# Kernel optimization log

Measured on AMD Instinct MI355X. Metric: run time of the kernel, lower is better.

Reference implementation:

```python
import jax, jax.numpy as jnp
import numpy as np

D_MODEL = 1024
N_HEADS = 16
HEAD_DIM = D_MODEL // N_HEADS
D_FF = 4096
B, T = 2, 2048


def layernorm(x, g, b, eps=1e-5):
    mu = jnp.mean(x, axis=-1, keepdims=True)
    var = jnp.var(x, axis=-1, keepdims=True)
    return (x - mu) * jax.lax.rsqrt(var + eps) * g + b


def setup_inputs() -> dict:
    key = jax.random.key(0)
    ks = jax.random.split(key, 8)
    s = 0.02
    return {
        "x": jax.random.normal(ks[0], (B, T, D_MODEL), dtype=jnp.float32),
        "ln1_g": jnp.ones((D_MODEL,), jnp.float32),
        "ln1_b": jnp.zeros((D_MODEL,), jnp.float32),
        "qkv_w": jax.random.normal(ks[1], (D_MODEL, 3 * D_MODEL), jnp.float32) * s,
        "qkv_b": jnp.zeros((3 * D_MODEL,), jnp.float32),
        "proj_w": jax.random.normal(ks[2], (D_MODEL, D_MODEL), jnp.float32) * s,
        "proj_b": jnp.zeros((D_MODEL,), jnp.float32),
        "ln2_g": jnp.ones((D_MODEL,), jnp.float32),
        "ln2_b": jnp.zeros((D_MODEL,), jnp.float32),
        "mlp_w1": jax.random.normal(ks[3], (D_MODEL, D_FF), jnp.float32) * s,
        "mlp_b1": jnp.zeros((D_FF,), jnp.float32),
        "mlp_w2": jax.random.normal(ks[4], (D_FF, D_MODEL), jnp.float32) * s,
        "mlp_b2": jnp.zeros((D_MODEL,), jnp.float32),
    }


def reference(x, ln1_g, ln1_b, qkv_w, qkv_b, proj_w, proj_b,
              ln2_g, ln2_b, mlp_w1, mlp_b1, mlp_w2, mlp_b2):
    Bv, Tv, C = x.shape
    scale = HEAD_DIM ** -0.5
    # --- attention branch ---
    h = layernorm(x, ln1_g, ln1_b)
    qkv = h @ qkv_w + qkv_b                                   # [B,T,3C]
    qkv = qkv.reshape(Bv, Tv, 3, N_HEADS, HEAD_DIM)
    q, k, v = qkv[:, :, 0], qkv[:, :, 1], qkv[:, :, 2]        # [B,T,H,Dh]
    att = jnp.einsum('bqhd,bkhd->bhqk', q, k) * scale         # [B,H,T,T]
    causal = jnp.tril(jnp.ones((Tv, Tv), dtype=bool))
    att = jnp.where(causal[None, None], att, -jnp.inf)
    att = jax.nn.softmax(att, axis=-1)
    out = jnp.einsum('bhqk,bkhd->bqhd', att, v).reshape(Bv, Tv, C)
    out = out @ proj_w + proj_b
    x = x + out
    # --- mlp branch ---
    h2 = layernorm(x, ln2_g, ln2_b)
    h2 = jax.nn.gelu(h2 @ mlp_w1 + mlp_b1, approximate=False)
    x = x + (h2 @ mlp_w2 + mlp_b2)
    return x
```

## Files before the change

kernel.cpp:

```cpp
#include <hip/hip_runtime.h>
#include <hip/hip_bf16.h>
#include <cstdint>

typedef __attribute__((ext_vector_type(4))) float f32x4;
typedef __attribute__((ext_vector_type(8))) __bf16 bf16x8;
typedef __attribute__((ext_vector_type(4))) __bf16 bf16x4;

#define EPI_BF16 0
#define EPI_GELU 1
#define EPI_RES  2

__device__ __forceinline__ void gll16(const void* g, void* l) {
  __builtin_amdgcn_global_load_lds((__attribute__((address_space(1))) void*)(g),
                                   (__attribute__((address_space(3))) void*)(l), 16, 0, 0);
}

__global__ __launch_bounds__(256)
void convT(const float* __restrict__ W, __bf16* __restrict__ WT, int Kd, int Nd)
{
  __shared__ __bf16 t[64][72];
  const int tid = threadIdx.x;
  const int n0 = blockIdx.x * 64, k0 = blockIdx.y * 64;
#pragma unroll
  for (int i = 0; i < 4; ++i) {
    const int c = i * 256 + tid;
    const int r = c >> 4, cc = (c & 15) * 4;
    const float4 v = *(const float4*)(W + (size_t)(k0 + r) * Nd + n0 + cc);
    bf16x4 tv; tv[0] = (__bf16)v.x; tv[1] = (__bf16)v.y; tv[2] = (__bf16)v.z; tv[3] = (__bf16)v.w;
    *(bf16x4*)&t[r][cc] = tv;
  }
  __syncthreads();
#pragma unroll
  for (int i = 0; i < 2; ++i) {
    const int c = i * 256 + tid;
    const int n = c >> 3, s = (c & 7) * 8;
    bf16x8 o;
#pragma unroll
    for (int j = 0; j < 8; ++j) o[j] = t[s + j][n];
    *(bf16x8*)(WT + (size_t)(n0 + n) * Kd + k0 + s) = o;
  }
}

__global__ __launch_bounds__(256)
void ln_rows(const float* __restrict__ x, const float* __restrict__ g,
             const float* __restrict__ b, __bf16* __restrict__ out)
{
  const int row = blockIdx.x;
  const int tid = threadIdx.x;
  const float4 v = *(const float4*)(x + (size_t)row * 1024 + tid * 4);
  float s = v.x + v.y + v.z + v.w;
  float q = v.x * v.x + v.y * v.y + v.z * v.z + v.w * v.w;
#pragma unroll
  for (int o = 32; o; o >>= 1) { s += __shfl_xor(s, o); q += __shfl_xor(q, o); }
  __shared__ float red[8];
  const int wid = tid >> 6;
  if ((tid & 63) == 0) { red[wid] = s; red[4 + wid] = q; }
  __syncthreads();
  s = red[0] + red[1] + red[2] + red[3];
  q = red[4] + red[5] + red[6] + red[7];
  const float mu = s * (1.0f / 1024.0f);
  const float var = q * (1.0f / 1024.0f) - mu * mu;
  const float rs = rsqrtf(var + 1e-5f);
  bf16x4 o4;
#pragma unroll
  for (int i = 0; i < 4; ++i) {
    const int c = tid * 4 + i;
    const float xv = (&v.x)[i];
    o4[i] = (__bf16)((xv - mu) * rs * g[c] + b[c]);
  }
  *(bf16x4*)(out + (size_t)row * 1024 + tid * 4) = o4;
}

template<int EPI>
__global__ __launch_bounds__(256)
void gemm_bt(const __bf16* __restrict__ A, const __bf16* __restrict__ BT,
             const float* __restrict__ bias, const float* __restrict__ R,
             void* __restrict__ Out, int M, int N, int K)
{
  const int tid = threadIdx.x;
  const int lane = tid & 63, wid = tid >> 6;
  const int l15 = lane & 15, lg = lane >> 4;
  const int wm = (wid >> 1) * 64, wn = (wid & 1) * 64;
  const int rowBase = blockIdx.y * 128, colBase = blockIdx.x * 128;
  __shared__ __bf16 As[128 * 32];
  __shared__ __bf16 Bs[128 * 32];
  f32x4 acc[4][4] = {};

  for (int k0 = 0; k0 < K; k0 += 32) {
#pragma unroll
    for (int i = 0; i < 2; ++i) {
      const int c = i * 256 + tid;
      const int r = c >> 2, s = (c & 3) * 8;
      gll16(A + (size_t)(rowBase + r) * K + (k0 + s), As + c * 8);
    }
#pragma unroll
    for (int i = 0; i < 2; ++i) {
      const int c = i * 256 + tid;
      const int r = c >> 2, s = (c & 3) * 8;
      gll16(BT + (size_t)(colBase + r) * K + (k0 + s), Bs + c * 8);
    }
    __syncthreads();
    bf16x8 af[4], bfr[4];
#pragma unroll
    for (int m = 0; m < 4; ++m) af[m] = *(const bf16x8*)(As + (wm + m * 16 + l15) * 32 + lg * 8);
#pragma unroll
    for (int n = 0; n < 4; ++n) bfr[n] = *(const bf16x8*)(Bs + (wn + n * 16 + l15) * 32 + lg * 8);
#pragma unroll
    for (int m = 0; m < 4; ++m)
#pragma unroll
      for (int n = 0; n < 4; ++n)
        acc[m][n] = __builtin_amdgcn_mfma_f32_16x16x32_bf16(af[m], bfr[n], acc[m][n], 0, 0, 0);
    __syncthreads();
  }
#pragma unroll
  for (int m = 0; m < 4; ++m) {
#pragma unroll
    for (int n = 0; n < 4; ++n) {
      const int col = colBase + wn + n * 16 + l15;
      const float bb = bias[col];
#pragma unroll
      for (int i = 0; i < 4; ++i) {
        const int row = rowBase + wm + m * 16 + lg * 4 + i;
        float v = acc[m][n][i] + bb;
        if constexpr (EPI == EPI_GELU) {
          v = 0.5f * v * (1.0f + erff(v * 0.70710678118654752f));
          ((__bf16*)Out)[(size_t)row * N + col] = (__bf16)v;
        } else if constexpr (EPI == EPI_BF16) {
          ((__bf16*)Out)[(size_t)row * N + col] = (__bf16)v;
        } else {
          v += R[(size_t)row * N + col];
          ((float*)Out)[(size_t)row * N + col] = v;
        }
      }
    }
  }
}

__global__ __launch_bounds__(256)
void rearrange(const __bf16* __restrict__ qkv, __bf16* __restrict__ Q,
               __bf16* __restrict__ Kb, __bf16* __restrict__ VT)
{
  __shared__ __bf16 vt[64][72];
  const int tid = threadIdx.x;
  const int bid = blockIdx.x;
  const int bh = bid >> 5, tt = bid & 31;
  const int b = bh >> 4, h = bh & 15;
  const int t0 = tt * 64;
#pragma unroll
  for (int i = 0; i < 2; ++i) {
    const int c = i * 256 + tid;
    const int tk = c >> 3, d0 = (c & 7) * 8;
    const size_t srow = (size_t)(b * 2048 + t0 + tk) * 3072 + h * 64 + d0;
    const size_t drow = (size_t)(bh * 2048 + t0 + tk) * 64 + d0;
    *(bf16x8*)(Q + drow) = *(const bf16x8*)(qkv + srow);
    *(bf16x8*)(Kb + drow) = *(const bf16x8*)(qkv + srow + 1024);
    *(bf16x8*)&vt[tk][d0] = *(const bf16x8*)(qkv + srow + 2048);
  }
  __syncthreads();
#pragma unroll
  for (int i = 0; i < 2; ++i) {
    const int c = i * 256 + tid;
    const int d = c >> 3, s = (c & 7) * 8;
    bf16x8 o;
#pragma unroll
    for (int j = 0; j < 8; ++j) o[j] = vt[s + j][d];
    *(bf16x8*)(VT + (size_t)(bh * 64 + d) * 2048 + t0 + s) = o;
  }
}

__global__ __launch_bounds__(256)
void attn(const __bf16* __restrict__ Q, const __bf16* __restrict__ K,
          const __bf16* __restrict__ VT, __bf16* __restrict__ O)
{
  const int bid = blockIdx.x;
  const int bh = bid >> 5, qt = bid & 31;
  const int tid = threadIdx.x;
  const int lane = tid & 63, w = tid >> 6;
  const int l15 = lane & 15, lg = lane >> 4;
  __shared__ __bf16 Ks[64 * 64];
  __shared__ __bf16 Vs[64 * 64];
  __shared__ __bf16 Ps[4][16 * 72];
  const size_t base = (size_t)bh * 2048 * 64;
  const int qrow0 = qt * 64 + w * 16;
  bf16x8 aq[2];
#pragma unroll
  for (int kk = 0; kk < 2; ++kk)
    aq[kk] = *(const bf16x8*)(Q + base + (size_t)(qrow0 + l15) * 64 + kk * 32 + lg * 8);
  f32x4 oacc[4] = {};
  float mst[4], lst[4];
#pragma unroll
  for (int i = 0; i < 4; ++i) { mst[i] = -INFINITY; lst[i] = 0.0f; }

  const int xsw = (l15 & 7) << 3;

  for (int j = 0; j <= qt; ++j) {
#pragma unroll
    for (int i = 0; i < 2; ++i) {
      const int c = i * 256 + tid;
      const int r = c >> 3;
      const int sc = ((c & 7) ^ (r & 7)) * 8;
      gll16(K + base + (size_t)(j * 64 + r) * 64 + sc, Ks + c * 8);
      gll16(VT + base + (size_t)r * 2048 + j * 64 + sc, Vs + c * 8);
    }
    __syncthreads();
    f32x4 sf[4];
#pragma unroll
    for (int n = 0; n < 4; ++n) {
      f32x4 z = {};
#pragma unroll
      for (int kk = 0; kk < 2; ++kk) {
        bf16x8 bk = *(const bf16x8*)(Ks + (n * 16 + l15) * 64 + ((kk * 32 + lg * 8) ^ xsw));
        z = __builtin_amdgcn_mfma_f32_16x16x32_bf16(aq[kk], bk, z, 0, 0, 0);
      }
      sf[n] = z;
    }
    const bool diag = (j == qt);
#pragma unroll
    for (int n = 0; n < 4; ++n)
#pragma unroll
      for (int i = 0; i < 4; ++i) {
        float sv = sf[n][i] * 0.125f;
        if (diag) {
          const int kv = j * 64 + n * 16 + l15;
          const int qr = qrow0 + lg * 4 + i;
          if (kv > qr) sv = -INFINITY;
        }
        sf[n][i] = sv;
      }
    float mx[4], cf[4], rsum[4];
#pragma unroll
    for (int i = 0; i < 4; ++i) {
      float t = fmaxf(fmaxf(sf[0][i], sf[1][i]), fmaxf(sf[2][i], sf[3][i]));
#pragma unroll
      for (int o = 1; o < 16; o <<= 1) t = fmaxf(t, __shfl_xor(t, o));
      mx[i] = fmaxf(t, mst[i]);
      cf[i] = __expf(mst[i] - mx[i]);
      rsum[i] = 0.0f;
    }
#pragma unroll
    for (int n = 0; n < 4; ++n)
#pragma unroll
      for (int i = 0; i < 4; ++i) {
        const float p = __expf(sf[n][i] - mx[i]);
        rsum[i] += p;
        Ps[w][(lg * 4 + i) * 72 + n * 16 + l15] = (__bf16)p;
      }
#pragma unroll
    for (int i = 0; i < 4; ++i) {
      float t = rsum[i];
#pragma unroll
      for (int o = 1; o < 16; o <<= 1) t += __shfl_xor(t, o);
      lst[i] = lst[i] * cf[i] + t;
      mst[i] = mx[i];
    }
#pragma unroll
    for (int n = 0; n < 4; ++n)
#pragma unroll
      for (int i = 0; i < 4; ++i) oacc[n][i] *= cf[i];
#pragma unroll
    for (int t = 0; t < 2; ++t) {
      bf16x8 ap = *(const bf16x8*)(Ps[w] + l15 * 72 + t * 32 + lg * 8);
#pragma unroll
      for (int n = 0; n < 4; ++n) {
        bf16x8 bv = *(const bf16x8*)(Vs + (n * 16 + l15) * 64 + ((t * 32 + lg * 8) ^ xsw));
        oacc[n] = __builtin_amdgcn_mfma_f32_16x16x32_bf16(ap, bv, oacc[n], 0, 0, 0);
      }
    }
    __syncthreads();
  }
  const int b = bh >> 4, h = bh & 15;
#pragma unroll
  for (int i = 0; i < 4; ++i) {
    const float inv = 1.0f / lst[i];
    const int t = qrow0 + lg * 4 + i;
#pragma unroll
    for (int n = 0; n < 4; ++n)
      O[(size_t)(b * 2048 + t) * 1024 + h * 64 + n * 16 + l15] = (__bf16)(oacc[n][i] * inv);
  }
}

extern "C" void kernel_launch(void* const* d_in, const int* in_sizes, int n_in,
                              void* d_out, int out_size, void* d_ws, size_t ws_size,
                              hipStream_t stream)
{
  const float* x      = (const float*)d_in[0];
  const float* ln1_g  = (const float*)d_in[1];
  const float* ln1_b  = (const float*)d_in[2];
  const float* qkv_w  = (const float*)d_in[3];
  const float* qkv_b  = (const float*)d_in[4];
  const float* proj_w = (const float*)d_in[5];
  const float* proj_b = (const float*)d_in[6];
  const float* ln2_g  = (const float*)d_in[7];
  const float* ln2_b  = (const float*)d_in[8];
  const float* mlp_w1 = (const float*)d_in[9];
  const float* mlp_b1 = (const float*)d_in[10];
  const float* mlp_w2 = (const float*)d_in[11];
  const float* mlp_b2 = (const float*)d_in[12];

  char* ws = (char*)d_ws;
  __bf16* qkvT  = (__bf16*)(ws + 0);
  __bf16* projT = (__bf16*)(ws + 6291456);
  __bf16* w1T   = (__bf16*)(ws + 8388608);
  __bf16* w2T   = (__bf16*)(ws + 16777216);
  __bf16* h1    = (__bf16*)(ws + 25165824);
  __bf16* qkv   = (__bf16*)(ws + 33554432);
  __bf16* act1  = (__bf16*)(ws + 33554432);
  __bf16* Qb    = (__bf16*)(ws + 58720256);
  __bf16* Kb    = (__bf16*)(ws + 67108864);
  __bf16* VTb   = (__bf16*)(ws + 75497472);
  __bf16* attO  = (__bf16*)(ws + 83886080);
  float*  x2    = (float*) (ws + 92274688);
  __bf16* h2    = (__bf16*)(ws + 109051904);

  convT<<<dim3(48, 16), 256, 0, stream>>>(qkv_w, qkvT, 1024, 3072);
  convT<<<dim3(16, 16), 256, 0, stream>>>(proj_w, projT, 1024, 1024);
  convT<<<dim3(64, 16), 256, 0, stream>>>(mlp_w1, w1T, 1024, 4096);
  convT<<<dim3(16, 64), 256, 0, stream>>>(mlp_w2, w2T, 4096, 1024);

  ln_rows<<<4096, 256, 0, stream>>>(x, ln1_g, ln1_b, h1);
  gemm_bt<EPI_BF16><<<dim3(24, 32), 256, 0, stream>>>(h1, qkvT, qkv_b, nullptr, qkv, 4096, 3072, 1024);
  rearrange<<<1024, 256, 0, stream>>>(qkv, Qb, Kb, VTb);
  attn<<<1024, 256, 0, stream>>>(Qb, Kb, VTb, attO);
  gemm_bt<EPI_RES><<<dim3(8, 32), 256, 0, stream>>>(attO, projT, proj_b, x, x2, 4096, 1024, 1024);
  ln_rows<<<4096, 256, 0, stream>>>(x2, ln2_g, ln2_b, h2);
  gemm_bt<EPI_GELU><<<dim3(32, 32), 256, 0, stream>>>(h2, w1T, mlp_b1, nullptr, act1, 4096, 4096, 1024);
  gemm_bt<EPI_RES><<<dim3(8, 32), 256, 0, stream>>>(act1, w2T, mlp_b2, x2, (float*)d_out, 4096, 1024, 4096);
}
```

Baseline: 485.8 us.

## Rewrite attention with 32x32 MFMA, transposed scores and register-resident P

The attention kernel now uses 2 waves of 32 query rows each with 32x32x16 bf16 MFMAs, computing S^T so each lane owns one query row. The softmax max and sum need only a single cross-half shuffle. P stays in registers via packed bf16 conversion and permlane32_swap instead of round-tripping through LDS. Blocks are also issued in reverse query-tile order so the longest causal tiles start first. The aim is to cut LDS traffic, shuffle reductions and instruction count, at the cost of fewer threads per block, more registers per lane, and correctness depending on the exact MFMA lane layout.

```diff
diff --git a/kernel.cpp b/kernel.cpp
--- a/kernel.cpp
+++ b/kernel.cpp
@@ -3,8 +3,11 @@
 #include <cstdint>
 
 typedef __attribute__((ext_vector_type(4))) float f32x4;
+typedef __attribute__((ext_vector_type(16))) float f32x16;
 typedef __attribute__((ext_vector_type(8))) __bf16 bf16x8;
 typedef __attribute__((ext_vector_type(4))) __bf16 bf16x4;
+typedef __attribute__((ext_vector_type(4))) uint32_t u32x4;
+typedef __attribute__((ext_vector_type(2))) unsigned int u32x2;
 
 #define EPI_BF16 0
 #define EPI_GELU 1
@@ -168,114 +171,118 @@
   }
 }
 
-__global__ __launch_bounds__(256)
+__global__ __launch_bounds__(128)
 void attn(const __bf16* __restrict__ Q, const __bf16* __restrict__ K,
           const __bf16* __restrict__ VT, __bf16* __restrict__ O)
 {
   const int bid = blockIdx.x;
-  const int bh = bid >> 5, qt = bid & 31;
+  const int bh = bid >> 5, qt = 31 - (bid & 31);
   const int tid = threadIdx.x;
   const int lane = tid & 63, w = tid >> 6;
-  const int l15 = lane & 15, lg = lane >> 4;
+  const int l31 = lane & 31, hi = lane >> 5;
   __shared__ __bf16 Ks[64 * 64];
   __shared__ __bf16 Vs[64 * 64];
-  __shared__ __bf16 Ps[4][16 * 72];
   const size_t base = (size_t)bh * 2048 * 64;
-  const int qrow0 = qt * 64 + w * 16;
-  bf16x8 aq[2];
-#pragma unroll
-  for (int kk = 0; kk < 2; ++kk)
-    aq[kk] = *(const bf16x8*)(Q + base + (size_t)(qrow0 + l15) * 64 + kk * 32 + lg * 8);
-  f32x4 oacc[4] = {};
-  float mst[4], lst[4];
-#pragma unroll
-  for (int i = 0; i < 4; ++i) { mst[i] = -INFINITY; lst[i] = 0.0f; }
-
-  const int xsw = (l15 & 7) << 3;
+  const int qrow0 = qt * 64 + w * 32;
+  const int xsw = (l31 & 7) << 3;
+
+  bf16x8 qf[4];
+#pragma unroll
+  for (int s = 0; s < 4; ++s)
+    qf[s] = *(const bf16x8*)(Q + base + (size_t)(qrow0 + l31) * 64 + s * 16 + hi * 8);
+
+  f32x16 oa0 = {}, oa1 = {};
+  float mst = -INFINITY, lst = 0.0f;
 
   for (int j = 0; j <= qt; ++j) {
 #pragma unroll
-    for (int i = 0; i < 2; ++i) {
-      const int c = i * 256 + tid;
+    for (int rnd = 0; rnd < 4; ++rnd) {
+      const int c = rnd * 128 + tid;
       const int r = c >> 3;
-      const int sc = ((c & 7) ^ (r & 7)) * 8;
-      gll16(K + base + (size_t)(j * 64 + r) * 64 + sc, Ks + c * 8);
-      gll16(VT + base + (size_t)r * 2048 + j * 64 + sc, Vs + c * 8);
+      const int e = ((c & 7) ^ (r & 7)) * 8;
+      gll16(K + base + (size_t)(j * 64 + r) * 64 + e, Ks + c * 8);
+      gll16(VT + base + (size_t)r * 2048 + j * 64 + e, Vs + c * 8);
     }
     __syncthreads();
-    f32x4 sf[4];
-#pragma unroll
-    for (int n = 0; n < 4; ++n) {
-      f32x4 z = {};
-#pragma unroll
-      for (int kk = 0; kk < 2; ++kk) {
-        bf16x8 bk = *(const bf16x8*)(Ks + (n * 16 + l15) * 64 + ((kk * 32 + lg * 8) ^ xsw));
-        z = __builtin_amdgcn_mfma_f32_16x16x32_bf16(aq[kk], bk, z, 0, 0, 0);
+
+    f32x16 s0v = {}, s1v = {};
+#pragma unroll
+    for (int s = 0; s < 4; ++s) {
+      const int co = (s * 16 + hi * 8) ^ xsw;
+      bf16x8 ak0 = *(const bf16x8*)(Ks + l31 * 64 + co);
+      bf16x8 ak1 = *(const bf16x8*)(Ks + (32 + l31) * 64 + co);
+      s0v = __builtin_amdgcn_mfma_f32_32x32x16_bf16(ak0, qf[s], s0v, 0, 0, 0);
+      s1v = __builtin_amdgcn_mfma_f32_32x32x16_bf16(ak1, qf[s], s1v, 0, 0, 0);
+    }
+#pragma unroll
+    for (int rg = 0; rg < 16; ++rg) { s0v[rg] *= 0.125f; s1v[rg] *= 0.125f; }
+    if (j == qt) {
+      const int qg = qrow0 + l31;
+#pragma unroll
+      for (int rg = 0; rg < 16; ++rg) {
+        const int kr = j * 64 + ((rg & 3) + 8 * (rg >> 2)) + 4 * hi;
+        if (kr > qg) s0v[rg] = -INFINITY;
+        if (kr + 32 > qg) s1v[rg] = -INFINITY;
       }
-      sf[n] = z;
-    }
-    const bool diag = (j == qt);
-#pragma unroll
-    for (int n = 0; n < 4; ++n)
-#pragma unroll
-      for (int i = 0; i < 4; ++i) {
-        float sv = sf[n][i] * 0.125f;
-        if (diag) {
-          const int kv = j * 64 + n * 16 + l15;
-          const int qr = qrow0 + lg * 4 + i;
-          if (kv > qr) sv = -INFINITY;
-        }
-        sf[n][i] = sv;
+    }
+    float mx = s0v[0];
+#pragma unroll
+    for (int rg = 1; rg < 16; ++rg) mx = fmaxf(mx, s0v[rg]);
+#pragma unroll
+    for (int rg = 0; rg < 16; ++rg) mx = fmaxf(mx, s1v[rg]);
+    mx = fmaxf(mx, __shfl_xor(mx, 32));
+    const float mnew = fmaxf(mst, mx);
+    const float cf = __expf(mst - mnew);
+    float rs = 0.0f;
+#pragma unroll
+    for (int rg = 0; rg < 16; ++rg) {
+      s0v[rg] = __expf(s0v[rg] - mnew); rs += s0v[rg];
+      s1v[rg] = __expf(s1v[rg] - mnew); rs += s1v[rg];
+    }
+    rs += __shfl_xor(rs, 32);
+    lst = lst * cf + rs;
+    mst = mnew;
+#pragma unroll
+    for (int rg = 0; rg < 16; ++rg) {
+      const float cb = __shfl(cf, (rg & 3) + 8 * (rg >> 2) + 4 * hi);
+      oa0[rg] *= cb; oa1[rg] *= cb;
+    }
+#pragma unroll
+    for (int s = 0; s < 4; ++s) {
+      const int br = (s & 1) * 8;
+      uint32_t wA0, wA1, wB0, wB1;
+      if (s < 2) {
+        asm("v_cvt_pk_bf16_f32 %0, %1, %2" : "=v"(wA0) : "v"(s0v[br + 0]), "v"(s0v[br + 1]));
+        asm("v_cvt_pk_bf16_f32 %0, %1, %2" : "=v"(wA1) : "v"(s0v[br + 2]), "v"(s0v[br + 3]));
+        asm("v_cvt_pk_bf16_f32 %0, %1, %2" : "=v"(wB0) : "v"(s0v[br + 4]), "v"(s0v[br + 5]));
+        asm("v_cvt_pk_bf16_f32 %0, %1, %2" : "=v"(wB1) : "v"(s0v[br + 6]), "v"(s0v[br + 7]));
+      } else {
+        asm("v_cvt_pk_bf16_f32 %0, %1, %2" : "=v"(wA0) : "v"(s1v[br + 0]), "v"(s1v[br + 1]));
+        asm("v_cvt_pk_bf16_f32 %0, %1, %2" : "=v"(wA1) : "v"(s1v[br + 2]), "v"(s1v[br + 3]));
+        asm("v_cvt_pk_bf16_f32 %0, %1, %2" : "=v"(wB0) : "v"(s1v[br + 4]), "v"(s1v[br + 5]));
+        asm("v_cvt_pk_bf16_f32 %0, %1, %2" : "=v"(wB1) : "v"(s1v[br + 6]), "v"(s1v[br + 7]));
       }
-    float mx[4], cf[4], rsum[4];
-#pragma unroll
-    for (int i = 0; i < 4; ++i) {
-      float t = fmaxf(fmaxf(sf[0][i], sf[1][i]), fmaxf(sf[2][i], sf[3][i]));
-#pragma unroll
-      for (int o = 1; o < 16; o <<= 1) t = fmaxf(t, __shfl_xor(t, o));
-      mx[i] = fmaxf(t, mst[i]);
-      cf[i] = __expf(mst[i] - mx[i]);
-      rsum[i] = 0.0f;
-    }
-#pragma unroll
-    for (int n = 0; n < 4; ++n)
-#pragma unroll
-      for (int i = 0; i < 4; ++i) {
-        const float p = __expf(sf[n][i] - mx[i]);
-        rsum[i] += p;
-        Ps[w][(lg * 4 + i) * 72 + n * 16 + l15] = (__bf16)p;
-      }
-#pragma unroll
-    for (int i = 0; i < 4; ++i) {
-      float t = rsum[i];
-#pragma unroll
-      for (int o = 1; o < 16; o <<= 1) t += __shfl_xor(t, o);
-      lst[i] = lst[i] * cf[i] + t;
-      mst[i] = mx[i];
-    }
-#pragma unroll
-    for (int n = 0; n < 4; ++n)
-#pragma unroll
-      for (int i = 0; i < 4; ++i) oacc[n][i] *= cf[i];
-#pragma unroll
-    for (int t = 0; t < 2; ++t) {
-      bf16x8 ap = *(const bf16x8*)(Ps[w] + l15 * 72 + t * 32 + lg * 8);
-#pragma unroll
-      for (int n = 0; n < 4; ++n) {
-        bf16x8 bv = *(const bf16x8*)(Vs + (n * 16 + l15) * 64 + ((t * 32 + lg * 8) ^ xsw));
-        oacc[n] = __builtin_amdgcn_mfma_f32_16x16x32_bf16(ap, bv, oacc[n], 0, 0, 0);
-      }
+      const u32x2 r0 = __builtin_amdgcn_permlane32_swap(wA0, wB0, false, false);
+      const u32x2 r1 = __builtin_amdgcn_permlane32_swap(wA1, wB1, false, false);
+      u32x4 uu; uu.x = r0.x; uu.y = r1.x; uu.z = r0.y; uu.w = r1.y;
+      const bf16x8 pa = __builtin_bit_cast(bf16x8, uu);
+      const int co = (s * 16 + hi * 8) ^ xsw;
+      bf16x8 bv0 = *(const bf16x8*)(Vs + l31 * 64 + co);
+      bf16x8 bv1 = *(const bf16x8*)(Vs + (32 + l31) * 64 + co);
+      oa0 = __builtin_amdgcn_mfma_f32_32x32x16_bf16(pa, bv0, oa0, 0, 0, 0);
+      oa1 = __builtin_amdgcn_mfma_f32_32x32x16_bf16(pa, bv1, oa1, 0, 0, 0);
     }
     __syncthreads();
   }
-  const int b = bh >> 4, h = bh & 15;
-#pragma unroll
-  for (int i = 0; i < 4; ++i) {
-    const float inv = 1.0f / lst[i];
-    const int t = qrow0 + lg * 4 + i;
-#pragma unroll
-    for (int n = 0; n < 4; ++n)
-      O[(size_t)(b * 2048 + t) * 1024 + h * 64 + n * 16 + l15] = (__bf16)(oacc[n][i] * inv);
+  const float inv = 1.0f / lst;
+  const int b = bh >> 4, hd = bh & 15;
+#pragma unroll
+  for (int rg = 0; rg < 16; ++rg) {
+    const int cr = (rg & 3) + 8 * (rg >> 2) + 4 * hi;
+    const float ib = __shfl(inv, cr);
+    const int qr = qrow0 + cr;
+    O[(size_t)(b * 2048 + qr) * 1024 + hd * 64 + l31]      = (__bf16)(oa0[rg] * ib);
+    O[(size_t)(b * 2048 + qr) * 1024 + hd * 64 + 32 + l31] = (__bf16)(oa1[rg] * ib);
   }
 }
 
@@ -320,7 +327,7 @@
   ln_rows<<<4096, 256, 0, stream>>>(x, ln1_g, ln1_b, h1);
   gemm_bt<EPI_BF16><<<dim3(24, 32), 256, 0, stream>>>(h1, qkvT, qkv_b, nullptr, qkv, 4096, 3072, 1024);
   rearrange<<<1024, 256, 0, stream>>>(qkv, Qb, Kb, VTb);
-  attn<<<1024, 256, 0, stream>>>(Qb, Kb, VTb, attO);
+  attn<<<1024, 128, 0, stream>>>(Qb, Kb, VTb, attO);
   gemm_bt<EPI_RES><<<dim3(8, 32), 256, 0, stream>>>(attO, projT, proj_b, x, x2, 4096, 1024, 1024);
   ln_rows<<<4096, 256, 0, stream>>>(x2, ln2_g, ln2_b, h2);
   gemm_bt<EPI_GELU><<<dim3(32, 32), 256, 0, stream>>>(h2, w1T, mlp_b1, nullptr, act1, 4096, 4096, 1024);
```

Result: faster. 443.6 us (-8.7%).
